# Performance work log

Measured on AMD Instinct MI355X. Metric: run time of the kernel, lower is better.

Reference implementation:

```python
import jax, jax.numpy as jnp
import numpy as np

NEG = -1e9  # finite mask value (avoids NaN rows for fully-masked queries)


def setup_inputs() -> dict:
    key = jax.random.key(0)
    kq, kk, kv, ks = jax.random.split(key, 4)
    B, H, N, E = 4, 8, 2048, 64
    Q = jax.random.normal(kq, (B, H, N, E), dtype=jnp.float32)
    K = jax.random.normal(kk, (B, H, N, E), dtype=jnp.float32)
    V = jax.random.normal(kv, (B, H, N, E), dtype=jnp.float32)
    seqlens = jax.random.randint(ks, (B,), 1, N + 1, dtype=jnp.int32)
    return {"Q": Q, "K": K, "V": V, "seqlens": seqlens}


def reference(Q, K, V, seqlens):
    # SparTA SeqlenDynamicSparseAttention: per-batch masked attention.
    # scores = Q @ K^T (no 1/sqrt(E) scaling inside the kernel; Q/K are
    # assumed to be already-projected), softmax over keys < seqlen[b],
    # output zeroed for query rows >= seqlen[b].
    B, H, N, E = Q.shape
    pos = jnp.arange(N)
    valid = pos[None, :] < seqlens[:, None]  # [B, N] bool
    scores = jnp.einsum('bhqe,bhke->bhqk', Q, K)  # [B,H,N,N]
    scores = jnp.where(valid[:, None, None, :], scores, NEG)
    probs = jax.nn.softmax(scores, axis=-1)
    out = jnp.einsum('bhqk,bhke->bhqe', probs, V)  # [B,H,N,E]
    out = jnp.where(valid[:, None, :, None], out, 0.0)
    return out
```

## Files before the change

kernel.cpp:

```cpp
#include <hip/hip_runtime.h>

using f32x4  = __attribute__((ext_vector_type(4))) float;
using h16x2  = __attribute__((ext_vector_type(2))) _Float16;
using h16x4  = __attribute__((ext_vector_type(4))) _Float16;
using h16x8  = __attribute__((ext_vector_type(8))) _Float16;
using fp16x2 = __attribute__((ext_vector_type(2))) __fp16;

#define NEGBIG (-1e30f)
#define LOG2E  1.44269504f

__device__ inline h16x8 cvt8(f32x4 x, f32x4 y) {
    union { h16x8 v; fp16x2 p[4]; } u;
    u.p[0] = __builtin_amdgcn_cvt_pkrtz(x[0], x[1]);
    u.p[1] = __builtin_amdgcn_cvt_pkrtz(x[2], x[3]);
    u.p[2] = __builtin_amdgcn_cvt_pkrtz(y[0], y[1]);
    u.p[3] = __builtin_amdgcn_cvt_pkrtz(y[2], y[3]);
    return u.v;
}

__launch_bounds__(512)
__global__ void attn_kernel(const float* __restrict__ Qg,
                            const float* __restrict__ Kg,
                            const float* __restrict__ Vg,
                            const int*   __restrict__ seqlens,
                            float*       __restrict__ Og)
{
    constexpr int N = 2048, E = 64;
    const int qblk = blockIdx.x;
    const int bh   = blockIdx.y;
    const int b    = bh >> 3;
    const int seqlen = seqlens[b];
    const int qstart = qblk * 128;
    const int tid = threadIdx.x;

    float* Ob = Og + ((size_t)bh * N + qstart) * E;

    if (qstart >= seqlen) {
        f32x4 z = {0.f, 0.f, 0.f, 0.f};
        f32x4* op = (f32x4*)Ob;
        #pragma unroll
        for (int i = 0; i < 4; ++i) op[tid + i * 512] = z;
        return;
    }

    const float* Qb = Qg + (size_t)bh * N * E;
    const float* Kb = Kg + (size_t)bh * N * E;
    const float* Vb = Vg + (size_t)bh * N * E;

    __shared__ __attribute__((aligned(16))) _Float16 Ksh[64 * 64];
    __shared__ __attribute__((aligned(16))) _Float16 Vsh[64 * 64];

    const int wid  = tid >> 6;
    const int qsub = wid >> 2;
    const int widq = wid & 3;
    const int lane = tid & 63;
    const int lg   = lane >> 4;
    const int l16  = lane & 15;

    const bool active = (qstart + qsub * 64) < seqlen;

    const int qrow = qstart + qsub * 64 + widq * 16 + l16;
    h16x8 Qf[2];
    #pragma unroll
    for (int es = 0; es < 2; ++es) {
        const f32x4* qp = (const f32x4*)(Qb + (size_t)qrow * E + es * 32 + lg * 8);
        f32x4 x = qp[0] * LOG2E, y = qp[1] * LOG2E;
        Qf[es] = cvt8(x, y);
    }

    const int rK  = tid >> 3;
    const int cK  = tid & 7;
    const int vkey = tid & 63;
    const int ve0  = (tid >> 6) * 8;

    float m = NEGBIG, L = 0.f;
    f32x4 Ot[4] = {{0,0,0,0},{0,0,0,0},{0,0,0,0},{0,0,0,0}};

    auto loadStage = [&](int ks, f32x4& k0, f32x4& k1, f32x4& v0, f32x4& v1) {
        const f32x4* kp = (const f32x4*)(Kb + (size_t)(ks + rK) * E + cK * 8);
        k0 = kp[0]; k1 = kp[1];
        const f32x4* vp = (const f32x4*)(Vb + (size_t)(ks + vkey) * E + ve0);
        v0 = vp[0]; v1 = vp[1];
    };

    auto writeStage = [&](const f32x4& k0, const f32x4& k1,
                          const f32x4& v0, const f32x4& v1) {
        *(h16x8*)&Ksh[rK * 64 + ((cK ^ (rK & 7)) << 3)] = cvt8(k0, k1);
        float vv[8] = {v0[0], v0[1], v0[2], v0[3], v1[0], v1[1], v1[2], v1[3]};
        #pragma unroll
        for (int i = 0; i < 8; ++i) {
            int e = ve0 + i;
            Vsh[e * 64 + (((vkey >> 2) ^ (i << 1)) << 2) + (vkey & 3)] =
                (_Float16)vv[i];
        }
    };

    auto computeTile = [&](int ks) {
        if (!active) return;
        f32x4 St[4];
        #pragma unroll
        for (int kt = 0; kt < 4; ++kt) {
            f32x4 acc = {0, 0, 0, 0};
            int key = kt * 16 + l16;
            #pragma unroll
            for (int es = 0; es < 2; ++es) {
                int c = es * 4 + lg;
                h16x8 kf = *(const h16x8*)&Ksh[key * 64 + ((c ^ (key & 7)) << 3)];
                acc = __builtin_amdgcn_mfma_f32_16x16x32_f16(kf, Qf[es], acc, 0, 0, 0);
            }
            St[kt] = acc;
        }
        if (ks + 64 > seqlen) {
            #pragma unroll
            for (int kt = 0; kt < 4; ++kt) {
                int kb0 = ks + kt * 16 + lg * 4;
                #pragma unroll
                for (int j = 0; j < 4; ++j)
                    if (kb0 + j >= seqlen) St[kt][j] = NEGBIG;
            }
        }
        float tm = NEGBIG;
        #pragma unroll
        for (int kt = 0; kt < 4; ++kt)
            #pragma unroll
            for (int j = 0; j < 4; ++j) tm = fmaxf(tm, St[kt][j]);
        tm = fmaxf(tm, __shfl_xor(tm, 16));
        tm = fmaxf(tm, __shfl_xor(tm, 32));

        if (__any(tm > m + 8.f)) {
            float mn = fmaxf(m, tm);
            float sc = __builtin_amdgcn_exp2f(m - mn);
            m = mn;
            L *= sc;
            #pragma unroll
            for (int et = 0; et < 4; ++et) Ot[et] *= sc;
        }

        float ps = 0.f;
        h16x4 Pf[4];
        #pragma unroll
        for (int kt = 0; kt < 4; ++kt) {
            float p0 = __builtin_amdgcn_exp2f(St[kt][0] - m);
            float p1 = __builtin_amdgcn_exp2f(St[kt][1] - m);
            float p2 = __builtin_amdgcn_exp2f(St[kt][2] - m);
            float p3 = __builtin_amdgcn_exp2f(St[kt][3] - m);
            ps += (p0 + p1) + (p2 + p3);
            union { h16x4 v; fp16x2 p[2]; } u;
            u.p[0] = __builtin_amdgcn_cvt_pkrtz(p0, p1);
            u.p[1] = __builtin_amdgcn_cvt_pkrtz(p2, p3);
            Pf[kt] = u.v;
        }
        ps += __shfl_xor(ps, 16);
        ps += __shfl_xor(ps, 32);
        L += ps;

        #pragma unroll
        for (int kt = 0; kt < 4; ++kt) {
            #pragma unroll
            for (int et = 0; et < 4; ++et) {
                int e  = et * 16 + l16;
                int c8 = kt * 4 + lg;
                h16x4 vf = *(const h16x4*)&Vsh[e * 64 + ((c8 ^ ((e & 7) << 1)) << 2)];
                Ot[et] = __builtin_amdgcn_mfma_f32_16x16x16f16(vf, Pf[kt], Ot[et], 0, 0, 0);
            }
        }
    };

    f32x4 kA0, kA1, vA0, vA1, kB0, kB1, vB0, vB1;
    loadStage(0, kA0, kA1, vA0, vA1);
    int ks = 0;
    while (true) {
        __syncthreads();
        writeStage(kA0, kA1, vA0, vA1);
        if (ks + 64 < seqlen) loadStage(ks + 64, kB0, kB1, vB0, vB1);
        __syncthreads();
        computeTile(ks);
        ks += 64;
        if (ks >= seqlen) break;

        __syncthreads();
        writeStage(kB0, kB1, vB0, vB1);
        if (ks + 64 < seqlen) loadStage(ks + 64, kA0, kA1, vA0, vA1);
        __syncthreads();
        computeTile(ks);
        ks += 64;
        if (ks >= seqlen) break;
    }

    float invL = 1.f / L;
    float* orow = Ob + (size_t)(qsub * 64 + widq * 16 + l16) * E;
    if (qrow < seqlen) {
        #pragma unroll
        for (int et = 0; et < 4; ++et) {
            f32x4 o = Ot[et] * invL;
            *(f32x4*)(orow + et * 16 + lg * 4) = o;
        }
    } else {
        f32x4 z = {0, 0, 0, 0};
        #pragma unroll
        for (int et = 0; et < 4; ++et)
            *(f32x4*)(orow + et * 16 + lg * 4) = z;
    }
}

extern "C" void kernel_launch(void* const* d_in, const int* in_sizes, int n_in,
                              void* d_out, int out_size, void* d_ws, size_t ws_size,
                              hipStream_t stream)
{
    const float* Q = (const float*)d_in[0];
    const float* K = (const float*)d_in[1];
    const float* V = (const float*)d_in[2];
    const int*   S = (const int*)d_in[3];
    float*       O = (float*)d_out;

    dim3 grid(2048 / 128, 4 * 8);
    attn_kernel<<<grid, 512, 0, stream>>>(Q, K, V, S, O);
}
```

Baseline: 131.9 us.

## Split key dimension across blocks with flash-decoding style partial reduce

```diff
diff --git a/kernel.cpp b/kernel.cpp
--- a/kernel.cpp
+++ b/kernel.cpp
@@ -8,6 +8,8 @@
 
 #define NEGBIG (-1e30f)
 #define LOG2E  1.44269504f
+
+constexpr int BH = 32, Nn = 2048, En = 64;
 
 __device__ inline h16x8 cvt8(f32x4 x, f32x4 y) {
     union { h16x8 v; fp16x2 p[4]; } u;
@@ -17,35 +19,35 @@
     u.p[3] = __builtin_amdgcn_cvt_pkrtz(y[2], y[3]);
     return u.v;
 }
+__device__ inline h16x4 cvt4(f32x4 x) {
+    union { h16x4 v; fp16x2 p[2]; } u;
+    u.p[0] = __builtin_amdgcn_cvt_pkrtz(x[0], x[1]);
+    u.p[1] = __builtin_amdgcn_cvt_pkrtz(x[2], x[3]);
+    return u.v;
+}
 
 __launch_bounds__(512)
-__global__ void attn_kernel(const float* __restrict__ Qg,
-                            const float* __restrict__ Kg,
-                            const float* __restrict__ Vg,
-                            const int*   __restrict__ seqlens,
-                            float*       __restrict__ Og)
+__global__ void attn_part(const float* __restrict__ Qg,
+                          const float* __restrict__ Kg,
+                          const float* __restrict__ Vg,
+                          const int*   __restrict__ seqlens,
+                          _Float16*    __restrict__ Opart,
+                          float*       __restrict__ Wpart,
+                          int chunk)
 {
-    constexpr int N = 2048, E = 64;
     const int qblk = blockIdx.x;
     const int bh   = blockIdx.y;
-    const int b    = bh >> 3;
-    const int seqlen = seqlens[b];
+    const int s    = blockIdx.z;
+    const int seqlen = seqlens[bh >> 3];
     const int qstart = qblk * 128;
+    const int kbeg   = s * chunk;
+    if (qstart >= seqlen || kbeg >= seqlen) return;
+    const int kend = min(seqlen, kbeg + chunk);
+
+    const float* Qb = Qg + (size_t)bh * Nn * En;
+    const float* Kb = Kg + (size_t)bh * Nn * En;
+    const float* Vb = Vg + (size_t)bh * Nn * En;
     const int tid = threadIdx.x;
-
-    float* Ob = Og + ((size_t)bh * N + qstart) * E;
-
-    if (qstart >= seqlen) {
-        f32x4 z = {0.f, 0.f, 0.f, 0.f};
-        f32x4* op = (f32x4*)Ob;
-        #pragma unroll
-        for (int i = 0; i < 4; ++i) op[tid + i * 512] = z;
-        return;
-    }
-
-    const float* Qb = Qg + (size_t)bh * N * E;
-    const float* Kb = Kg + (size_t)bh * N * E;
-    const float* Vb = Vg + (size_t)bh * N * E;
 
     __shared__ __attribute__((aligned(16))) _Float16 Ksh[64 * 64];
     __shared__ __attribute__((aligned(16))) _Float16 Vsh[64 * 64];
@@ -56,20 +58,19 @@
     const int lane = tid & 63;
     const int lg   = lane >> 4;
     const int l16  = lane & 15;
-
     const bool active = (qstart + qsub * 64) < seqlen;
 
     const int qrow = qstart + qsub * 64 + widq * 16 + l16;
     h16x8 Qf[2];
     #pragma unroll
     for (int es = 0; es < 2; ++es) {
-        const f32x4* qp = (const f32x4*)(Qb + (size_t)qrow * E + es * 32 + lg * 8);
+        const f32x4* qp = (const f32x4*)(Qb + (size_t)qrow * En + es * 32 + lg * 8);
         f32x4 x = qp[0] * LOG2E, y = qp[1] * LOG2E;
         Qf[es] = cvt8(x, y);
     }
 
-    const int rK  = tid >> 3;
-    const int cK  = tid & 7;
+    const int rK   = tid >> 3;
+    const int cK   = tid & 7;
     const int vkey = tid & 63;
     const int ve0  = (tid >> 6) * 8;
 
@@ -77,12 +78,11 @@
     f32x4 Ot[4] = {{0,0,0,0},{0,0,0,0},{0,0,0,0},{0,0,0,0}};
 
     auto loadStage = [&](int ks, f32x4& k0, f32x4& k1, f32x4& v0, f32x4& v1) {
-        const f32x4* kp = (const f32x4*)(Kb + (size_t)(ks + rK) * E + cK * 8);
+        const f32x4* kp = (const f32x4*)(Kb + (size_t)(ks + rK) * En + cK * 8);
         k0 = kp[0]; k1 = kp[1];
-        const f32x4* vp = (const f32x4*)(Vb + (size_t)(ks + vkey) * E + ve0);
+        const f32x4* vp = (const f32x4*)(Vb + (size_t)(ks + vkey) * En + ve0);
         v0 = vp[0]; v1 = vp[1];
     };
-
     auto writeStage = [&](const f32x4& k0, const f32x4& k1,
                           const f32x4& v0, const f32x4& v1) {
         *(h16x8*)&Ksh[rK * 64 + ((cK ^ (rK & 7)) << 3)] = cvt8(k0, k1);
@@ -94,7 +94,6 @@
                 (_Float16)vv[i];
         }
     };
-
     auto computeTile = [&](int ks) {
         if (!active) return;
         f32x4 St[4];
@@ -130,12 +129,10 @@
         if (__any(tm > m + 8.f)) {
             float mn = fmaxf(m, tm);
             float sc = __builtin_amdgcn_exp2f(m - mn);
-            m = mn;
-            L *= sc;
+            m = mn; L *= sc;
             #pragma unroll
             for (int et = 0; et < 4; ++et) Ot[et] *= sc;
         }
-
         float ps = 0.f;
         h16x4 Pf[4];
         #pragma unroll
@@ -153,7 +150,6 @@
         ps += __shfl_xor(ps, 16);
         ps += __shfl_xor(ps, 32);
         L += ps;
-
         #pragma unroll
         for (int kt = 0; kt < 4; ++kt) {
             #pragma unroll
@@ -167,6 +163,208 @@
     };
 
     f32x4 kA0, kA1, vA0, vA1, kB0, kB1, vB0, vB1;
+    loadStage(kbeg, kA0, kA1, vA0, vA1);
+    int ks = kbeg;
+    while (true) {
+        __syncthreads();
+        writeStage(kA0, kA1, vA0, vA1);
+        if (ks + 64 < kend) loadStage(ks + 64, kB0, kB1, vB0, vB1);
+        __syncthreads();
+        computeTile(ks);
+        ks += 64;
+        if (ks >= kend) break;
+
+        __syncthreads();
+        writeStage(kB0, kB1, vB0, vB1);
+        if (ks + 64 < kend) loadStage(ks + 64, kA0, kA1, vA0, vA1);
+        __syncthreads();
+        computeTile(ks);
+        ks += 64;
+        if (ks >= kend) break;
+    }
+
+    if (active && qrow < seqlen) {
+        float lw = m + __log2f(L);
+        const size_t rbase = ((size_t)s * BH + bh) * Nn + qrow;
+        if (lg == 0) Wpart[rbase] = lw;
+        float invL = 1.f / L;
+        _Float16* op = Opart + rbase * En;
+        #pragma unroll
+        for (int et = 0; et < 4; ++et) {
+            f32x4 o = Ot[et] * invL;
+            *(h16x4*)&op[et * 16 + lg * 4] = cvt4(o);
+        }
+    }
+}
+
+__launch_bounds__(256)
+__global__ void reduce_k(const _Float16* __restrict__ Opart,
+                         const float*    __restrict__ Wpart,
+                         const int*      __restrict__ seqlens,
+                         float*          __restrict__ Og,
+                         int cshift)
+{
+    const int tid  = threadIdx.x;
+    const int r    = tid >> 3;
+    const int e8   = tid & 7;
+    const int grow = blockIdx.x * 32 + r;
+    const int bh   = grow >> 11;
+    const int row  = grow & (Nn - 1);
+    const int seqlen = seqlens[bh >> 3];
+
+    f32x4 a0 = {0, 0, 0, 0}, a1 = {0, 0, 0, 0};
+    if (row < seqlen) {
+        const int chunk = 1 << cshift;
+        const int nlive = (seqlen + chunk - 1) >> cshift;
+        float W = NEGBIG;
+        for (int s = 0; s < nlive; ++s)
+            W = fmaxf(W, Wpart[((size_t)s * BH + bh) * Nn + row]);
+        float denom = 0.f;
+        for (int s = 0; s < nlive; ++s) {
+            const size_t rbase = ((size_t)s * BH + bh) * Nn + row;
+            float a = __builtin_amdgcn_exp2f(Wpart[rbase] - W);
+            denom += a;
+            h16x8 o = *(const h16x8*)&Opart[rbase * En + e8 * 8];
+            a0[0] += a * (float)o[0]; a0[1] += a * (float)o[1];
+            a0[2] += a * (float)o[2]; a0[3] += a * (float)o[3];
+            a1[0] += a * (float)o[4]; a1[1] += a * (float)o[5];
+            a1[2] += a * (float)o[6]; a1[3] += a * (float)o[7];
+        }
+        float sc = 1.f / denom;
+        a0 *= sc; a1 *= sc;
+    }
+    float* op = Og + ((size_t)bh * Nn + row) * En + e8 * 8;
+    *(f32x4*)op       = a0;
+    *(f32x4*)(op + 4) = a1;
+}
+
+__launch_bounds__(512)
+__global__ void attn_kernel(const float* __restrict__ Qg,
+                            const float* __restrict__ Kg,
+                            const float* __restrict__ Vg,
+                            const int*   __restrict__ seqlens,
+                            float*       __restrict__ Og)
+{
+    const int qblk = blockIdx.x;
+    const int bh   = blockIdx.y;
+    const int seqlen = seqlens[bh >> 3];
+    const int qstart = qblk * 128;
+    const int tid = threadIdx.x;
+    float* Ob = Og + ((size_t)bh * Nn + qstart) * En;
+    if (qstart >= seqlen) {
+        f32x4 z = {0.f, 0.f, 0.f, 0.f};
+        f32x4* op = (f32x4*)Ob;
+        #pragma unroll
+        for (int i = 0; i < 4; ++i) op[tid + i * 512] = z;
+        return;
+    }
+    const float* Qb = Qg + (size_t)bh * Nn * En;
+    const float* Kb = Kg + (size_t)bh * Nn * En;
+    const float* Vb = Vg + (size_t)bh * Nn * En;
+    __shared__ __attribute__((aligned(16))) _Float16 Ksh[64 * 64];
+    __shared__ __attribute__((aligned(16))) _Float16 Vsh[64 * 64];
+    const int wid  = tid >> 6;
+    const int qsub = wid >> 2;
+    const int widq = wid & 3;
+    const int lane = tid & 63;
+    const int lg   = lane >> 4;
+    const int l16  = lane & 15;
+    const bool active = (qstart + qsub * 64) < seqlen;
+    const int qrow = qstart + qsub * 64 + widq * 16 + l16;
+    h16x8 Qf[2];
+    #pragma unroll
+    for (int es = 0; es < 2; ++es) {
+        const f32x4* qp = (const f32x4*)(Qb + (size_t)qrow * En + es * 32 + lg * 8);
+        f32x4 x = qp[0] * LOG2E, y = qp[1] * LOG2E;
+        Qf[es] = cvt8(x, y);
+    }
+    const int rK = tid >> 3, cK = tid & 7, vkey = tid & 63, ve0 = (tid >> 6) * 8;
+    float m = NEGBIG, L = 0.f;
+    f32x4 Ot[4] = {{0,0,0,0},{0,0,0,0},{0,0,0,0},{0,0,0,0}};
+    auto loadStage = [&](int ks, f32x4& k0, f32x4& k1, f32x4& v0, f32x4& v1) {
+        const f32x4* kp = (const f32x4*)(Kb + (size_t)(ks + rK) * En + cK * 8);
+        k0 = kp[0]; k1 = kp[1];
+        const f32x4* vp = (const f32x4*)(Vb + (size_t)(ks + vkey) * En + ve0);
+        v0 = vp[0]; v1 = vp[1];
+    };
+    auto writeStage = [&](const f32x4& k0, const f32x4& k1,
+                          const f32x4& v0, const f32x4& v1) {
+        *(h16x8*)&Ksh[rK * 64 + ((cK ^ (rK & 7)) << 3)] = cvt8(k0, k1);
+        float vv[8] = {v0[0], v0[1], v0[2], v0[3], v1[0], v1[1], v1[2], v1[3]};
+        #pragma unroll
+        for (int i = 0; i < 8; ++i) {
+            int e = ve0 + i;
+            Vsh[e * 64 + (((vkey >> 2) ^ (i << 1)) << 2) + (vkey & 3)] =
+                (_Float16)vv[i];
+        }
+    };
+    auto computeTile = [&](int ks) {
+        if (!active) return;
+        f32x4 St[4];
+        #pragma unroll
+        for (int kt = 0; kt < 4; ++kt) {
+            f32x4 acc = {0, 0, 0, 0};
+            int key = kt * 16 + l16;
+            #pragma unroll
+            for (int es = 0; es < 2; ++es) {
+                int c = es * 4 + lg;
+                h16x8 kf = *(const h16x8*)&Ksh[key * 64 + ((c ^ (key & 7)) << 3)];
+                acc = __builtin_amdgcn_mfma_f32_16x16x32_f16(kf, Qf[es], acc, 0, 0, 0);
+            }
+            St[kt] = acc;
+        }
+        if (ks + 64 > seqlen) {
+            #pragma unroll
+            for (int kt = 0; kt < 4; ++kt) {
+                int kb0 = ks + kt * 16 + lg * 4;
+                #pragma unroll
+                for (int j = 0; j < 4; ++j)
+                    if (kb0 + j >= seqlen) St[kt][j] = NEGBIG;
+            }
+        }
+        float tm = NEGBIG;
+        #pragma unroll
+        for (int kt = 0; kt < 4; ++kt)
+            #pragma unroll
+            for (int j = 0; j < 4; ++j) tm = fmaxf(tm, St[kt][j]);
+        tm = fmaxf(tm, __shfl_xor(tm, 16));
+        tm = fmaxf(tm, __shfl_xor(tm, 32));
+        if (__any(tm > m + 8.f)) {
+            float mn = fmaxf(m, tm);
+            float sc = __builtin_amdgcn_exp2f(m - mn);
+            m = mn; L *= sc;
+            #pragma unroll
+            for (int et = 0; et < 4; ++et) Ot[et] *= sc;
+        }
+        float ps = 0.f;
+        h16x4 Pf[4];
+        #pragma unroll
+        for (int kt = 0; kt < 4; ++kt) {
+            float p0 = __builtin_amdgcn_exp2f(St[kt][0] - m);
+            float p1 = __builtin_amdgcn_exp2f(St[kt][1] - m);
+            float p2 = __builtin_amdgcn_exp2f(St[kt][2] - m);
+            float p3 = __builtin_amdgcn_exp2f(St[kt][3] - m);
+            ps += (p0 + p1) + (p2 + p3);
+            union { h16x4 v; fp16x2 p[2]; } u;
+            u.p[0] = __builtin_amdgcn_cvt_pkrtz(p0, p1);
+            u.p[1] = __builtin_amdgcn_cvt_pkrtz(p2, p3);
+            Pf[kt] = u.v;
+        }
+        ps += __shfl_xor(ps, 16);
+        ps += __shfl_xor(ps, 32);
+        L += ps;
+        #pragma unroll
+        for (int kt = 0; kt < 4; ++kt) {
+            #pragma unroll
+            for (int et = 0; et < 4; ++et) {
+                int e  = et * 16 + l16;
+                int c8 = kt * 4 + lg;
+                h16x4 vf = *(const h16x4*)&Vsh[e * 64 + ((c8 ^ ((e & 7) << 1)) << 2)];
+                Ot[et] = __builtin_amdgcn_mfma_f32_16x16x16f16(vf, Pf[kt], Ot[et], 0, 0, 0);
+            }
+        }
+    };
+    f32x4 kA0, kA1, vA0, vA1, kB0, kB1, vB0, vB1;
     loadStage(0, kA0, kA1, vA0, vA1);
     int ks = 0;
     while (true) {
@@ -177,7 +375,6 @@
         computeTile(ks);
         ks += 64;
         if (ks >= seqlen) break;
-
         __syncthreads();
         writeStage(kB0, kB1, vB0, vB1);
         if (ks + 64 < seqlen) loadStage(ks + 64, kA0, kA1, vA0, vA1);
@@ -186,9 +383,8 @@
         ks += 64;
         if (ks >= seqlen) break;
     }
-
     float invL = 1.f / L;
-    float* orow = Ob + (size_t)(qsub * 64 + widq * 16 + l16) * E;
+    float* orow = Ob + (size_t)(qsub * 64 + widq * 16 + l16) * En;
     if (qrow < seqlen) {
         #pragma unroll
         for (int et = 0; et < 4; ++et) {
@@ -207,12 +403,31 @@
                               void* d_out, int out_size, void* d_ws, size_t ws_size,
                               hipStream_t stream)
 {
-    const float* Q = (const float*)d_in[0];
-    const float* K = (const float*)d_in[1];
-    const float* V = (const float*)d_in[2];
-    const int*   S = (const int*)d_in[3];
-    float*       O = (float*)d_out;
-
-    dim3 grid(2048 / 128, 4 * 8);
-    attn_kernel<<<grid, 512, 0, stream>>>(Q, K, V, S, O);
-}
+    const float* Q  = (const float*)d_in[0];
+    const float* K  = (const float*)d_in[1];
+    const float* V  = (const float*)d_in[2];
+    const int*   SL = (const int*)d_in[3];
+    float*       O  = (float*)d_out;
+
+    auto need = [](int S) {
+        return (size_t)S * BH * Nn * En * sizeof(_Float16)
+             + (size_t)S * BH * Nn * sizeof(float);
+    };
+    int S = 0;
+    if      (ws_size >= need(4)) S = 4;
+    else if (ws_size >= need(2)) S = 2;
+
+    if (S) {
+        _Float16* Opart = (_Float16*)d_ws;
+        float*    Wpart = (float*)((char*)d_ws
+                            + (size_t)S * BH * Nn * En * sizeof(_Float16));
+        const int chunk  = Nn / S;
+        const int cshift = (S == 4) ? 9 : 10;
+        attn_part<<<dim3(Nn / 128, BH, S), 512, 0, stream>>>(
+            Q, K, V, SL, Opart, Wpart, chunk);
+        reduce_k<<<dim3(BH * Nn / 32), 256, 0, stream>>>(
+            Opart, Wpart, SL, O, cshift);
+    } else {
+        attn_kernel<<<dim3(Nn / 128, BH), 512, 0, stream>>>(Q, K, V, SL, O);
+    }
+}
```

Result: slower. 136.3 us (+3.4%).
